# Performance work log

Hardware: AMD Instinct MI355X
Metric: run time of the kernel (lower is better)

The kernel has to match this reference:

```python
import jax, jax.numpy as jnp
import numpy as np

N = 50000
E = 800000
IN_DIM, HID_DIM, LAT_DIM, OUT_DIM = 128, 128, 64, 128
NEG_SLOPE = 0.2  # PyG GATConv default


def setup_inputs() -> dict:
    key = jax.random.key(0)
    ks = jax.random.split(key, 24)
    def glorot(k, shape):
        lim = float(np.sqrt(6.0 / (shape[0] + shape[-1])))
        return jax.random.uniform(k, shape, jnp.float32, -lim, lim)
    inp = {
        "x": jax.random.normal(ks[0], (N, IN_DIM), jnp.float32),
        "edge_index": jax.random.randint(ks[1], (2, E), 0, N, jnp.int32),
        "eps": jax.random.normal(ks[2], (N, LAT_DIM), jnp.float32),
        # GATConv 1 (heads=1)
        "W1": glorot(ks[3], (IN_DIM, HID_DIM)),
        "a_src1": glorot(ks[4], (HID_DIM,)),
        "a_dst1": glorot(ks[5], (HID_DIM,)),
        "b1": jnp.zeros((HID_DIM,), jnp.float32),
        # GATConv 2
        "W2": glorot(ks[6], (HID_DIM, LAT_DIM)),
        "a_src2": glorot(ks[7], (LAT_DIM,)),
        "a_dst2": glorot(ks[8], (LAT_DIM,)),
        "b2": jnp.zeros((LAT_DIM,), jnp.float32),
        # VAE heads
        "W_mu": glorot(ks[9], (LAT_DIM, LAT_DIM)),
        "b_mu": jnp.zeros((LAT_DIM,), jnp.float32),
        "W_lv": glorot(ks[10], (LAT_DIM, LAT_DIM)),
        "b_lv": jnp.zeros((LAT_DIM,), jnp.float32),
        "W_d1": glorot(ks[11], (LAT_DIM, HID_DIM)),
        "b_d1": jnp.zeros((HID_DIM,), jnp.float32),
        "W_d2": glorot(ks[12], (HID_DIM, OUT_DIM)),
        "b_d2": jnp.zeros((OUT_DIM,), jnp.float32),
    }
    return inp


def gat_conv(x, W, a_src, a_dst, b, src, dst):
    # x: [N, F_in] -> h: [N, F_out]
    h = x @ W
    # per-node attention halves (single head)
    alpha_s = h @ a_src           # [N]
    alpha_d = h @ a_dst           # [N]
    # per-edge score: leaky_relu(a_src . h_j + a_dst . h_i), edge j->i
    e = jax.nn.leaky_relu(alpha_s[src] + alpha_d[dst], NEG_SLOPE)  # [E']
    # scatter-softmax over incoming edges of each destination node
    m = jax.ops.segment_max(e, dst, num_segments=N)                # [N]
    ex = jnp.exp(e - m[dst])
    denom = jax.ops.segment_sum(ex, dst, num_segments=N)           # [N]
    w = ex / denom[dst]                                            # [E']
    # scatter-add weighted messages
    out = jax.ops.segment_sum(h[src] * w[:, None], dst, num_segments=N)
    return out + b


def reference(x, edge_index, eps, W1, a_src1, a_dst1, b1, W2, a_src2, a_dst2, b2,
              W_mu, b_mu, W_lv, b_lv, W_d1, b_d1, W_d2, b_d2):
    # add self loops (PyG GATConv default add_self_loops=True)
    loops = jnp.arange(N, dtype=edge_index.dtype)
    src = jnp.concatenate([edge_index[0], loops])
    dst = jnp.concatenate([edge_index[1], loops])

    h = jax.nn.relu(gat_conv(x, W1, a_src1, a_dst1, b1, src, dst))
    h = jax.nn.relu(gat_conv(h, W2, a_src2, a_dst2, b2, src, dst))
    mu = h @ W_mu + b_mu
    logvar = h @ W_lv + b_lv
    z = mu + eps * jnp.exp(0.5 * logvar)
    d = jax.nn.relu(z @ W_d1 + b_d1)
    recon_x = jax.nn.sigmoid(d @ W_d2 + b_d2)
    return recon_x, mu, logvar
```

## Files before the change

### kernel.cpp

```cpp
#include <hip/hip_runtime.h>
#include <stdint.h>

typedef unsigned int u32;

__device__ __forceinline__ float lrelu(float x){ return x > 0.f ? x : 0.2f*x; }

__global__ void k_hist(const int* __restrict__ dst, int* __restrict__ deg, int E){
  int e = blockIdx.x*blockDim.x + threadIdx.x;
  if (e < E) atomicAdd(&deg[dst[e]], 1);
}

__global__ void k_scan1(const int* __restrict__ deg, int* __restrict__ offs,
                        int* __restrict__ bsum, int n){
  __shared__ int lds[256];
  int t = threadIdx.x;
  int base = blockIdx.x*1024 + t*4;
  int v0 = (base+0<n)?deg[base+0]:0;
  int v1 = (base+1<n)?deg[base+1]:0;
  int v2 = (base+2<n)?deg[base+2]:0;
  int v3 = (base+3<n)?deg[base+3]:0;
  int s = v0+v1+v2+v3;
  lds[t] = s; __syncthreads();
  for (int off=1; off<256; off<<=1){
    int tmp = (t>=off)? lds[t-off] : 0;
    __syncthreads();
    lds[t] += tmp;
    __syncthreads();
  }
  int excl = lds[t] - s;
  if (t==255) bsum[blockIdx.x] = lds[255];
  if (base+0<n) offs[base+0] = excl;
  if (base+1<n) offs[base+1] = excl+v0;
  if (base+2<n) offs[base+2] = excl+v0+v1;
  if (base+3<n) offs[base+3] = excl+v0+v1+v2;
}

__global__ void k_scan2(int* bsum, int nb){
  int lane = threadIdx.x;
  int v = (lane<nb)? bsum[lane] : 0;
  int orig = v;
  for (int off=1; off<64; off<<=1){
    int t = __shfl_up(v, off);
    if (lane >= off) v += t;
  }
  if (lane<nb) bsum[lane] = v - orig;
}

__global__ void k_scan3(int* __restrict__ offs, int* __restrict__ cur,
                        const int* __restrict__ bsum, int n){
  int i = blockIdx.x*blockDim.x + threadIdx.x;
  if (i<n){ int v = offs[i] + bsum[i>>10]; offs[i]=v; cur[i]=v; }
}

__global__ void k_scatter(const int* __restrict__ src, const int* __restrict__ dst,
                          int* __restrict__ cur, int* __restrict__ adj, int E){
  int e = blockIdx.x*blockDim.x + threadIdx.x;
  if (e<E){
    int d = dst[e];
    int p = atomicAdd(&cur[d], 1);
    adj[p] = src[e];
  }
}

template<int FOUT>
__global__ __launch_bounds__(256) void k_gemm_t(const float* __restrict__ X,
                                                const float* __restrict__ W,
                                                float* __restrict__ H, int N){
  constexpr int CG = FOUT/4;
  constexpr int RG = 256/CG;
  constexpr int TR = RG*4;
  __shared__ float xs[TR*128];
  __shared__ float ws[128*FOUT];
  int t = threadIdx.x;
  long i0 = (long)blockIdx.x * TR;
  {
    constexpr int NV = TR*32/256;
    #pragma unroll
    for (int j=0;j<NV;j++){
      int idx = t + 256*j;
      int row = idx >> 5, c4 = idx & 31;
      float4 v = make_float4(0.f,0.f,0.f,0.f);
      if (i0 + row < N) v = *(const float4*)&X[(i0+row)*128 + c4*4];
      *(float4*)&xs[row*128 + c4*4] = v;
    }
  }
  {
    constexpr int NW = 128*FOUT/4/256;
    const float4* Wv = (const float4*)W;
    float4* wd = (float4*)ws;
    #pragma unroll
    for (int j=0;j<NW;j++) wd[t + 256*j] = Wv[t + 256*j];
  }
  __syncthreads();
  int ci = t & (CG-1), rg = t / CG;
  float4 a0 = make_float4(0,0,0,0), a1 = a0, a2 = a0, a3 = a0;
  const float* xrow = &xs[(rg*4)*128];
  #pragma unroll 8
  for (int k=0;k<128;k++){
    float4 w4 = *(const float4*)&ws[k*FOUT + ci*4];
    float x0 = xrow[k];
    float x1 = xrow[128 + k];
    float x2 = xrow[256 + k];
    float x3 = xrow[384 + k];
    a0.x = fmaf(x0, w4.x, a0.x); a0.y = fmaf(x0, w4.y, a0.y);
    a0.z = fmaf(x0, w4.z, a0.z); a0.w = fmaf(x0, w4.w, a0.w);
    a1.x = fmaf(x1, w4.x, a1.x); a1.y = fmaf(x1, w4.y, a1.y);
    a1.z = fmaf(x1, w4.z, a1.z); a1.w = fmaf(x1, w4.w, a1.w);
    a2.x = fmaf(x2, w4.x, a2.x); a2.y = fmaf(x2, w4.y, a2.y);
    a2.z = fmaf(x2, w4.z, a2.z); a2.w = fmaf(x2, w4.w, a2.w);
    a3.x = fmaf(x3, w4.x, a3.x); a3.y = fmaf(x3, w4.y, a3.y);
    a3.z = fmaf(x3, w4.z, a3.z); a3.w = fmaf(x3, w4.w, a3.w);
  }
  long ib = i0 + rg*4;
  if (ib+0 < N) *(float4*)&H[(ib+0)*FOUT + ci*4] = a0;
  if (ib+1 < N) *(float4*)&H[(ib+1)*FOUT + ci*4] = a1;
  if (ib+2 < N) *(float4*)&H[(ib+2)*FOUT + ci*4] = a2;
  if (ib+3 < N) *(float4*)&H[(ib+3)*FOUT + ci*4] = a3;
}

template<int F>
__global__ void k_alpha(const float* __restrict__ H, const float* __restrict__ Asrc,
                        const float* __restrict__ Adst, float* __restrict__ AS,
                        float* __restrict__ AD, int N){
  int lane = threadIdx.x & 63;
  int i = blockIdx.x*4 + (threadIdx.x >> 6);
  if (i >= N) return;
  float as = 0.f, ad = 0.f;
  #pragma unroll
  for (int c = lane; c < F; c += 64){
    float hv = H[(long)i*F + c];
    as = fmaf(hv, Asrc[c], as);
    ad = fmaf(hv, Adst[c], ad);
  }
  #pragma unroll
  for (int off=32; off; off>>=1){
    as += __shfl_xor(as, off);
    ad += __shfl_xor(ad, off);
  }
  if (lane==0){ AS[i]=as; AD[i]=ad; }
}

template<int F>
__global__ void k_agg(const float* __restrict__ H, const float* __restrict__ AS,
                      const float* __restrict__ AD, const float* __restrict__ B,
                      const int* __restrict__ offs, const int* __restrict__ deg,
                      const int* __restrict__ adj, float* __restrict__ OUT, int N){
  int lane = threadIdx.x & 63;
  int i = blockIdx.x*4 + (threadIdx.x >> 6);
  if (i >= N) return;
  int start = offs[i], dg = deg[i];
  float ad = AD[i];
  float lr_self = lrelu(AS[i] + ad);
  float m = -1e30f, dacc = 0.f;
  for (int b0=0; b0<dg; b0+=64){
    int k = b0 + lane;
    if (k < dg){
      int s = adj[start+k];
      float lr = lrelu(AS[s] + ad);
      float mn = fmaxf(m, lr);
      dacc = dacc*__expf(m-mn) + __expf(lr-mn);
      m = mn;
    }
  }
  #pragma unroll
  for (int off=32; off; off>>=1){
    float m2 = __shfl_xor(m, off);
    float d2 = __shfl_xor(dacc, off);
    float mn = fmaxf(m, m2);
    dacc = dacc*__expf(m-mn) + d2*__expf(m2-mn);
    m = mn;
  }
  float M = fmaxf(m, lr_self);
  float D = dacc*__expf(m-M) + __expf(lr_self-M);
  float invD = 1.f/D;
  float wself = __expf(lr_self-M)*invD;
  float acc0 = wself * H[(long)i*F + lane];
  float acc1 = 0.f;
  if (F==128) acc1 = wself * H[(long)i*F + 64 + lane];
  for (int b0=0; b0<dg; b0+=64){
    int k = b0 + lane;
    int sreg = 0; float wreg = 0.f;
    if (k < dg){
      sreg = adj[start+k];
      wreg = __expf(lrelu(AS[sreg]+ad) - M)*invD;
    }
    int cnt = min(64, dg-b0);
    int kk = 0;
    for (; kk+4<=cnt; kk+=4){
      int   s0=__shfl(sreg,kk),   s1=__shfl(sreg,kk+1),   s2=__shfl(sreg,kk+2),   s3=__shfl(sreg,kk+3);
      float w0=__shfl(wreg,kk),   w1=__shfl(wreg,kk+1),   w2=__shfl(wreg,kk+2),   w3=__shfl(wreg,kk+3);
      float h0 = H[(long)s0*F+lane];
      float h1 = H[(long)s1*F+lane];
      float h2 = H[(long)s2*F+lane];
      float h3 = H[(long)s3*F+lane];
      acc0 += w0*h0 + w1*h1 + w2*h2 + w3*h3;
      if (F==128){
        float g0 = H[(long)s0*F+64+lane];
        float g1 = H[(long)s1*F+64+lane];
        float g2 = H[(long)s2*F+64+lane];
        float g3 = H[(long)s3*F+64+lane];
        acc1 += w0*g0 + w1*g1 + w2*g2 + w3*g3;
      }
    }
    for (; kk<cnt; kk++){
      int s0=__shfl(sreg,kk); float w0=__shfl(wreg,kk);
      acc0 += w0*H[(long)s0*F+lane];
      if (F==128) acc1 += w0*H[(long)s0*F+64+lane];
    }
  }
  float o0 = fmaxf(acc0 + B[lane], 0.f);
  OUT[(long)i*F+lane] = o0;
  if (F==128){
    float o1 = fmaxf(acc1 + B[64+lane], 0.f);
    OUT[(long)i*F+64+lane] = o1;
  }
}

__global__ __launch_bounds__(512) void k_head_t(
    const float* __restrict__ H2, const float* __restrict__ EPS,
    const float* __restrict__ Wmu, const float* __restrict__ bmu,
    const float* __restrict__ Wlv, const float* __restrict__ blv,
    const float* __restrict__ Wd1, const float* __restrict__ bd1,
    const float* __restrict__ Wd2, const float* __restrict__ bd2,
    float* __restrict__ out_recon, float* __restrict__ out_mu,
    float* __restrict__ out_lv, int N){
  __shared__ float hs[64*64];
  __shared__ float zs[64*64];
  __shared__ float dsb[64*128];
  __shared__ float ws[128*128];
  int t = threadIdx.x;
  long i0 = (long)blockIdx.x * 64;
  #pragma unroll
  for (int j=0;j<2;j++){
    int idx = t + 512*j;
    int row = idx >> 4, c4 = idx & 15;
    float4 v = make_float4(0.f,0.f,0.f,0.f);
    if (i0 + row < N) v = *(const float4*)&H2[(i0+row)*64 + c4*4];
    *(float4*)&hs[row*64 + c4*4] = v;
  }
  #pragma unroll
  for (int j=0;j<4;j++){
    int q = t + 512*j;
    int k = q >> 5, c4 = q & 31;
    float4 v;
    if (c4 < 16) v = *(const float4*)&Wmu[k*64 + c4*4];
    else         v = *(const float4*)&Wlv[k*64 + (c4-16)*4];
    *(float4*)&ws[k*128 + c4*4] = v;
  }
  __syncthreads();
  int ci = t & 31, rg = t >> 5;
  float4 a0 = make_float4(0,0,0,0), a1 = a0, a2 = a0, a3 = a0;
  {
    const float* xrow = &hs[(rg*4)*64];
    #pragma unroll 8
    for (int k=0;k<64;k++){
      float4 w4 = *(const float4*)&ws[k*128 + ci*4];
      float x0 = xrow[k], x1 = xrow[64+k], x2 = xrow[128+k], x3 = xrow[192+k];
      a0.x=fmaf(x0,w4.x,a0.x); a0.y=fmaf(x0,w4.y,a0.y); a0.z=fmaf(x0,w4.z,a0.z); a0.w=fmaf(x0,w4.w,a0.w);
      a1.x=fmaf(x1,w4.x,a1.x); a1.y=fmaf(x1,w4.y,a1.y); a1.z=fmaf(x1,w4.z,a1.z); a1.w=fmaf(x1,w4.w,a1.w);
      a2.x=fmaf(x2,w4.x,a2.x); a2.y=fmaf(x2,w4.y,a2.y); a2.z=fmaf(x2,w4.z,a2.z); a2.w=fmaf(x2,w4.w,a2.w);
      a3.x=fmaf(x3,w4.x,a3.x); a3.y=fmaf(x3,w4.y,a3.y); a3.z=fmaf(x3,w4.z,a3.z); a3.w=fmaf(x3,w4.w,a3.w);
    }
  }
  bool is_mu = (ci < 16);
  int cbase = is_mu ? ci*4 : (ci-16)*4;
  if (!is_mu){
    float4 bv = *(const float4*)&blv[cbase];
    float4 acc[4] = {a0,a1,a2,a3};
    #pragma unroll
    for (int r=0;r<4;r++){
      long i = i0 + rg*4 + r;
      float4 lv = make_float4(acc[r].x+bv.x, acc[r].y+bv.y, acc[r].z+bv.z, acc[r].w+bv.w);
      if (i < N) *(float4*)&out_lv[i*64 + cbase] = lv;
      *(float4*)&zs[(rg*4+r)*64 + cbase] = lv;
    }
  }
  __syncthreads();
  if (is_mu){
    float4 bv = *(const float4*)&bmu[cbase];
    float4 acc[4] = {a0,a1,a2,a3};
    #pragma unroll
    for (int r=0;r<4;r++){
      long i = i0 + rg*4 + r;
      float4 mu = make_float4(acc[r].x+bv.x, acc[r].y+bv.y, acc[r].z+bv.z, acc[r].w+bv.w);
      if (i < N) *(float4*)&out_mu[i*64 + cbase] = mu;
      float4 lv = *(const float4*)&zs[(rg*4+r)*64 + cbase];
      float4 e = make_float4(0.f,0.f,0.f,0.f);
      if (i < N) e = *(const float4*)&EPS[i*64 + cbase];
      float4 z;
      z.x = fmaf(e.x, __expf(0.5f*lv.x), mu.x);
      z.y = fmaf(e.y, __expf(0.5f*lv.y), mu.y);
      z.z = fmaf(e.z, __expf(0.5f*lv.z), mu.z);
      z.w = fmaf(e.w, __expf(0.5f*lv.w), mu.w);
      *(float4*)&zs[(rg*4+r)*64 + cbase] = z;
    }
  }
  {
    const float4* Wv = (const float4*)Wd1;
    float4* wd = (float4*)ws;
    #pragma unroll
    for (int j=0;j<4;j++) wd[t + 512*j] = Wv[t + 512*j];
  }
  __syncthreads();
  a0 = make_float4(0,0,0,0); a1 = a0; a2 = a0; a3 = a0;
  {
    const float* xrow = &zs[(rg*4)*64];
    #pragma unroll 8
    for (int k=0;k<64;k++){
      float4 w4 = *(const float4*)&ws[k*128 + ci*4];
      float x0 = xrow[k], x1 = xrow[64+k], x2 = xrow[128+k], x3 = xrow[192+k];
      a0.x=fmaf(x0,w4.x,a0.x); a0.y=fmaf(x0,w4.y,a0.y); a0.z=fmaf(x0,w4.z,a0.z); a0.w=fmaf(x0,w4.w,a0.w);
      a1.x=fmaf(x1,w4.x,a1.x); a1.y=fmaf(x1,w4.y,a1.y); a1.z=fmaf(x1,w4.z,a1.z); a1.w=fmaf(x1,w4.w,a1.w);
      a2.x=fmaf(x2,w4.x,a2.x); a2.y=fmaf(x2,w4.y,a2.y); a2.z=fmaf(x2,w4.z,a2.z); a2.w=fmaf(x2,w4.w,a2.w);
      a3.x=fmaf(x3,w4.x,a3.x); a3.y=fmaf(x3,w4.y,a3.y); a3.z=fmaf(x3,w4.z,a3.z); a3.w=fmaf(x3,w4.w,a3.w);
    }
  }
  __syncthreads();
  {
    float4 bv = *(const float4*)&bd1[ci*4];
    float4 acc[4] = {a0,a1,a2,a3};
    #pragma unroll
    for (int r=0;r<4;r++){
      float4 d;
      d.x = fmaxf(acc[r].x+bv.x, 0.f); d.y = fmaxf(acc[r].y+bv.y, 0.f);
      d.z = fmaxf(acc[r].z+bv.z, 0.f); d.w = fmaxf(acc[r].w+bv.w, 0.f);
      *(float4*)&dsb[(rg*4+r)*128 + ci*4] = d;
    }
  }
  {
    const float4* Wv = (const float4*)Wd2;
    float4* wd = (float4*)ws;
    #pragma unroll
    for (int j=0;j<8;j++) wd[t + 512*j] = Wv[t + 512*j];
  }
  __syncthreads();
  a0 = make_float4(0,0,0,0); a1 = a0; a2 = a0; a3 = a0;
  {
    const float* xrow = &dsb[(rg*4)*128];
    #pragma unroll 8
    for (int k=0;k<128;k++){
      float4 w4 = *(const float4*)&ws[k*128 + ci*4];
      float x0 = xrow[k], x1 = xrow[128+k], x2 = xrow[256+k], x3 = xrow[384+k];
      a0.x=fmaf(x0,w4.x,a0.x); a0.y=fmaf(x0,w4.y,a0.y); a0.z=fmaf(x0,w4.z,a0.z); a0.w=fmaf(x0,w4.w,a0.w);
      a1.x=fmaf(x1,w4.x,a1.x); a1.y=fmaf(x1,w4.y,a1.y); a1.z=fmaf(x1,w4.z,a1.z); a1.w=fmaf(x1,w4.w,a1.w);
      a2.x=fmaf(x2,w4.x,a2.x); a2.y=fmaf(x2,w4.y,a2.y); a2.z=fmaf(x2,w4.z,a2.z); a2.w=fmaf(x2,w4.w,a2.w);
      a3.x=fmaf(x3,w4.x,a3.x); a3.y=fmaf(x3,w4.y,a3.y); a3.z=fmaf(x3,w4.z,a3.z); a3.w=fmaf(x3,w4.w,a3.w);
    }
  }
  {
    float4 bv = *(const float4*)&bd2[ci*4];
    float4 acc[4] = {a0,a1,a2,a3};
    #pragma unroll
    for (int r=0;r<4;r++){
      long i = i0 + rg*4 + r;
      if (i < N){
        float4 o;
        o.x = 1.f/(1.f+__expf(-(acc[r].x+bv.x)));
        o.y = 1.f/(1.f+__expf(-(acc[r].y+bv.y)));
        o.z = 1.f/(1.f+__expf(-(acc[r].z+bv.z)));
        o.w = 1.f/(1.f+__expf(-(acc[r].w+bv.w)));
        *(float4*)&out_recon[i*128 + ci*4] = o;
      }
    }
  }
}

extern "C" void kernel_launch(void* const* d_in, const int* in_sizes, int n_in,
                              void* d_out, int out_size, void* d_ws, size_t ws_size,
                              hipStream_t stream){
  const float* x    = (const float*)d_in[0];
  const int*   ei   = (const int*)  d_in[1];
  const float* eps  = (const float*)d_in[2];
  const float* W1   = (const float*)d_in[3];
  const float* as1v = (const float*)d_in[4];
  const float* ad1v = (const float*)d_in[5];
  const float* b1   = (const float*)d_in[6];
  const float* W2   = (const float*)d_in[7];
  const float* as2v = (const float*)d_in[8];
  const float* ad2v = (const float*)d_in[9];
  const float* b2   = (const float*)d_in[10];
  const float* Wmu  = (const float*)d_in[11];
  const float* bmu  = (const float*)d_in[12];
  const float* Wlv  = (const float*)d_in[13];
  const float* blv  = (const float*)d_in[14];
  const float* Wd1  = (const float*)d_in[15];
  const float* bd1  = (const float*)d_in[16];
  const float* Wd2  = (const float*)d_in[17];
  const float* bd2  = (const float*)d_in[18];

  const int N = in_sizes[0] / 128;
  const int E = in_sizes[1] / 2;
  const int* esrc = ei;
  const int* edst = ei + E;

  char* wp = (char*)d_ws;
  auto alloc = [&](size_t bytes)->char*{
    char* p = wp; wp += (bytes + 255) & ~(size_t)255; return p;
  };
  int*   deg  = (int*)  alloc((size_t)N*4);
  int*   offs = (int*)  alloc((size_t)N*4);
  int*   cur  = (int*)  alloc((size_t)N*4);
  int*   bsum = (int*)  alloc(256*4);
  int*   adj  = (int*)  alloc((size_t)E*4);
  float* h1   = (float*)alloc((size_t)N*128*4);
  float* o1   = (float*)alloc((size_t)N*128*4);
  float* AS1  = (float*)alloc((size_t)N*4);
  float* AD1  = (float*)alloc((size_t)N*4);
  float* AS2  = (float*)alloc((size_t)N*4);
  float* AD2  = (float*)alloc((size_t)N*4);
  float* h2 = h1;
  float* o2 = h1 + (size_t)N*64;
  (void)ws_size; (void)n_in; (void)out_size;

  float* out_recon = (float*)d_out;
  float* out_mu    = out_recon + (size_t)N*128;
  float* out_lv    = out_mu    + (size_t)N*64;

  hipMemsetAsync(deg, 0, (size_t)N*4, stream);
  int eb = (E + 255)/256;
  int nb = (N + 1023)/1024;
  k_hist   <<<eb, 256, 0, stream>>>(edst, deg, E);
  k_scan1  <<<nb, 256, 0, stream>>>(deg, offs, bsum, N);
  k_scan2  <<<1,   64, 0, stream>>>(bsum, nb);
  k_scan3  <<<(N+255)/256, 256, 0, stream>>>(offs, cur, bsum, N);
  k_scatter<<<eb, 256, 0, stream>>>(esrc, edst, cur, adj, E);

  int wb  = (N+3)/4;
  int gb1 = (N+31)/32;
  int gb2 = (N+63)/64;
  int hb  = (N+63)/64;
  k_gemm_t<128><<<gb1, 256, 0, stream>>>(x, W1, h1, N);
  k_alpha<128> <<<wb, 256, 0, stream>>>(h1, as1v, ad1v, AS1, AD1, N);
  k_agg<128>   <<<wb, 256, 0, stream>>>(h1, AS1, AD1, b1, offs, deg, adj, o1, N);
  k_gemm_t<64> <<<gb2, 256, 0, stream>>>(o1, W2, h2, N);
  k_alpha<64>  <<<wb, 256, 0, stream>>>(h2, as2v, ad2v, AS2, AD2, N);
  k_agg<64>    <<<wb, 256, 0, stream>>>(h2, AS2, AD2, b2, offs, deg, adj, o2, N);
  k_head_t     <<<hb, 512, 0, stream>>>(o2, eps, Wmu, bmu, Wlv, blv, Wd1, bd1, Wd2, bd2,
                                        out_recon, out_mu, out_lv, N);
}
```

Before: 445.4 us.

## Fuse attention logits into GEMM, vectorize aggregation, drop LDS weight staging

The per-node attention dot products move into the GEMM epilogue through shuffle reductions, which removes both alpha kernels. The GEMMs and the head kernel now read weights straight from global or cache instead of staging them in LDS, and each thread computes more rows. Aggregation gains a single-pass softmax for nodes with degree up to 64 and processes several edges per wavefront with float4 lanes, reducing across lane partitions at the end. The trade-offs are higher register pressure and weight reads that now depend on cache behaviour.

```diff
diff --git a/kernel.cpp b/kernel.cpp
--- a/kernel.cpp
+++ b/kernel.cpp
@@ -62,161 +62,166 @@
   }
 }
 
-template<int FOUT>
-__global__ __launch_bounds__(256) void k_gemm_t(const float* __restrict__ X,
-                                                const float* __restrict__ W,
-                                                float* __restrict__ H, int N){
+template<int FOUT, int RPT>
+__global__ __launch_bounds__(256) void k_gemm2(const float* __restrict__ X,
+    const float* __restrict__ W, const float* __restrict__ Avs,
+    const float* __restrict__ Avd, float* __restrict__ H,
+    float* __restrict__ AS, float* __restrict__ AD, int N){
   constexpr int CG = FOUT/4;
   constexpr int RG = 256/CG;
-  constexpr int TR = RG*4;
+  constexpr int TR = RG*RPT;
   __shared__ float xs[TR*128];
-  __shared__ float ws[128*FOUT];
   int t = threadIdx.x;
   long i0 = (long)blockIdx.x * TR;
-  {
-    constexpr int NV = TR*32/256;
-    #pragma unroll
-    for (int j=0;j<NV;j++){
-      int idx = t + 256*j;
-      int row = idx >> 5, c4 = idx & 31;
-      float4 v = make_float4(0.f,0.f,0.f,0.f);
-      if (i0 + row < N) v = *(const float4*)&X[(i0+row)*128 + c4*4];
-      *(float4*)&xs[row*128 + c4*4] = v;
-    }
-  }
-  {
-    constexpr int NW = 128*FOUT/4/256;
-    const float4* Wv = (const float4*)W;
-    float4* wd = (float4*)ws;
-    #pragma unroll
-    for (int j=0;j<NW;j++) wd[t + 256*j] = Wv[t + 256*j];
+  #pragma unroll
+  for (int j=0;j<TR*128/4/256;j++){
+    int idx = t + 256*j;
+    int row = idx >> 5, c4 = idx & 31;
+    float4 v = make_float4(0.f,0.f,0.f,0.f);
+    if (i0 + row < N) v = *(const float4*)&X[(i0+row)*128 + c4*4];
+    *(float4*)&xs[row*128 + c4*4] = v;
   }
   __syncthreads();
   int ci = t & (CG-1), rg = t / CG;
-  float4 a0 = make_float4(0,0,0,0), a1 = a0, a2 = a0, a3 = a0;
-  const float* xrow = &xs[(rg*4)*128];
-  #pragma unroll 8
+  const float* Wc = W + ci*4;
+  float4 acc[RPT];
+  #pragma unroll
+  for (int r=0;r<RPT;r++) acc[r] = make_float4(0.f,0.f,0.f,0.f);
+  const float* xrow = &xs[(rg*RPT)*128];
+  #pragma unroll 4
   for (int k=0;k<128;k++){
-    float4 w4 = *(const float4*)&ws[k*FOUT + ci*4];
-    float x0 = xrow[k];
-    float x1 = xrow[128 + k];
-    float x2 = xrow[256 + k];
-    float x3 = xrow[384 + k];
-    a0.x = fmaf(x0, w4.x, a0.x); a0.y = fmaf(x0, w4.y, a0.y);
-    a0.z = fmaf(x0, w4.z, a0.z); a0.w = fmaf(x0, w4.w, a0.w);
-    a1.x = fmaf(x1, w4.x, a1.x); a1.y = fmaf(x1, w4.y, a1.y);
-    a1.z = fmaf(x1, w4.z, a1.z); a1.w = fmaf(x1, w4.w, a1.w);
-    a2.x = fmaf(x2, w4.x, a2.x); a2.y = fmaf(x2, w4.y, a2.y);
-    a2.z = fmaf(x2, w4.z, a2.z); a2.w = fmaf(x2, w4.w, a2.w);
-    a3.x = fmaf(x3, w4.x, a3.x); a3.y = fmaf(x3, w4.y, a3.y);
-    a3.z = fmaf(x3, w4.z, a3.z); a3.w = fmaf(x3, w4.w, a3.w);
-  }
-  long ib = i0 + rg*4;
-  if (ib+0 < N) *(float4*)&H[(ib+0)*FOUT + ci*4] = a0;
-  if (ib+1 < N) *(float4*)&H[(ib+1)*FOUT + ci*4] = a1;
-  if (ib+2 < N) *(float4*)&H[(ib+2)*FOUT + ci*4] = a2;
-  if (ib+3 < N) *(float4*)&H[(ib+3)*FOUT + ci*4] = a3;
+    float4 w4 = *(const float4*)&Wc[k*FOUT];
+    #pragma unroll
+    for (int r=0;r<RPT;r++){
+      float xv = xrow[r*128 + k];
+      acc[r].x = fmaf(xv, w4.x, acc[r].x);
+      acc[r].y = fmaf(xv, w4.y, acc[r].y);
+      acc[r].z = fmaf(xv, w4.z, acc[r].z);
+      acc[r].w = fmaf(xv, w4.w, acc[r].w);
+    }
+  }
+  float4 vs = *(const float4*)&Avs[ci*4];
+  float4 vd = *(const float4*)&Avd[ci*4];
+  float asv[RPT], adv[RPT];
+  #pragma unroll
+  for (int r=0;r<RPT;r++){
+    asv[r] = acc[r].x*vs.x + acc[r].y*vs.y + acc[r].z*vs.z + acc[r].w*vs.w;
+    adv[r] = acc[r].x*vd.x + acc[r].y*vd.y + acc[r].z*vd.z + acc[r].w*vd.w;
+  }
+  #pragma unroll
+  for (int off=1; off<CG; off<<=1){
+    #pragma unroll
+    for (int r=0;r<RPT;r++){
+      asv[r] += __shfl_xor(asv[r], off);
+      adv[r] += __shfl_xor(adv[r], off);
+    }
+  }
+  long rb = i0 + rg*RPT;
+  #pragma unroll
+  for (int r=0;r<RPT;r++)
+    if (rb + r < N) *(float4*)&H[(rb+r)*FOUT + ci*4] = acc[r];
+  if (ci == 0){
+    #pragma unroll
+    for (int r=0;r<RPT;r++)
+      if (rb + r < N){ AS[rb+r] = asv[r]; AD[rb+r] = adv[r]; }
+  }
 }
 
 template<int F>
-__global__ void k_alpha(const float* __restrict__ H, const float* __restrict__ Asrc,
-                        const float* __restrict__ Adst, float* __restrict__ AS,
-                        float* __restrict__ AD, int N){
-  int lane = threadIdx.x & 63;
-  int i = blockIdx.x*4 + (threadIdx.x >> 6);
-  if (i >= N) return;
-  float as = 0.f, ad = 0.f;
-  #pragma unroll
-  for (int c = lane; c < F; c += 64){
-    float hv = H[(long)i*F + c];
-    as = fmaf(hv, Asrc[c], as);
-    ad = fmaf(hv, Adst[c], ad);
-  }
-  #pragma unroll
-  for (int off=32; off; off>>=1){
-    as += __shfl_xor(as, off);
-    ad += __shfl_xor(ad, off);
-  }
-  if (lane==0){ AS[i]=as; AD[i]=ad; }
-}
-
-template<int F>
-__global__ void k_agg(const float* __restrict__ H, const float* __restrict__ AS,
-                      const float* __restrict__ AD, const float* __restrict__ B,
-                      const int* __restrict__ offs, const int* __restrict__ deg,
-                      const int* __restrict__ adj, float* __restrict__ OUT, int N){
+__global__ __launch_bounds__(256) void k_agg2(const float* __restrict__ H,
+    const float* __restrict__ AS, const float* __restrict__ AD,
+    const float* __restrict__ B, const int* __restrict__ offs,
+    const int* __restrict__ deg, const int* __restrict__ adj,
+    float* __restrict__ OUT, int N){
+  constexpr int PL = F/4;
+  constexpr int PARTS = 64/PL;
   int lane = threadIdx.x & 63;
   int i = blockIdx.x*4 + (threadIdx.x >> 6);
   if (i >= N) return;
   int start = offs[i], dg = deg[i];
   float ad = AD[i];
   float lr_self = lrelu(AS[i] + ad);
-  float m = -1e30f, dacc = 0.f;
+  int part = lane / PL, lp = lane % PL;
+  float M, invD, wfast = 0.f;
+  int sfast = i;
+  if (dg <= 64){
+    float lr = -1e30f;
+    if (lane < dg){ sfast = adj[start+lane]; lr = lrelu(AS[sfast] + ad); }
+    float m = lr;
+    #pragma unroll
+    for (int off=32; off; off>>=1) m = fmaxf(m, __shfl_xor(m, off));
+    M = fmaxf(m, lr_self);
+    float p = (lane < dg) ? __expf(lr - M) : 0.f;
+    float d = p;
+    #pragma unroll
+    for (int off=32; off; off>>=1) d += __shfl_xor(d, off);
+    invD = 1.f/(d + __expf(lr_self - M));
+    wfast = p * invD;
+  } else {
+    float m = -1e30f, dacc = 0.f;
+    for (int b0=0; b0<dg; b0+=64){
+      int k = b0 + lane;
+      if (k < dg){
+        int s = adj[start+k];
+        float lr = lrelu(AS[s] + ad);
+        float mn = fmaxf(m, lr);
+        dacc = dacc*__expf(m-mn) + __expf(lr-mn);
+        m = mn;
+      }
+    }
+    #pragma unroll
+    for (int off=32; off; off>>=1){
+      float m2 = __shfl_xor(m, off);
+      float d2 = __shfl_xor(dacc, off);
+      float mn = fmaxf(m, m2);
+      dacc = dacc*__expf(m-mn) + d2*__expf(m2-mn);
+      m = mn;
+    }
+    M = fmaxf(m, lr_self);
+    invD = 1.f/(dacc*__expf(m-M) + __expf(lr_self-M));
+  }
+  float4 acc = make_float4(0.f,0.f,0.f,0.f);
+  if (part == 0){
+    float ws_ = __expf(lr_self - M)*invD;
+    float4 hv = *(const float4*)&H[(long)i*F + lp*4];
+    acc.x = ws_*hv.x; acc.y = ws_*hv.y; acc.z = ws_*hv.z; acc.w = ws_*hv.w;
+  }
   for (int b0=0; b0<dg; b0+=64){
-    int k = b0 + lane;
-    if (k < dg){
-      int s = adj[start+k];
-      float lr = lrelu(AS[s] + ad);
-      float mn = fmaxf(m, lr);
-      dacc = dacc*__expf(m-mn) + __expf(lr-mn);
-      m = mn;
-    }
-  }
-  #pragma unroll
-  for (int off=32; off; off>>=1){
-    float m2 = __shfl_xor(m, off);
-    float d2 = __shfl_xor(dacc, off);
-    float mn = fmaxf(m, m2);
-    dacc = dacc*__expf(m-mn) + d2*__expf(m2-mn);
-    m = mn;
-  }
-  float M = fmaxf(m, lr_self);
-  float D = dacc*__expf(m-M) + __expf(lr_self-M);
-  float invD = 1.f/D;
-  float wself = __expf(lr_self-M)*invD;
-  float acc0 = wself * H[(long)i*F + lane];
-  float acc1 = 0.f;
-  if (F==128) acc1 = wself * H[(long)i*F + 64 + lane];
-  for (int b0=0; b0<dg; b0+=64){
-    int k = b0 + lane;
-    int sreg = 0; float wreg = 0.f;
-    if (k < dg){
-      sreg = adj[start+k];
-      wreg = __expf(lrelu(AS[sreg]+ad) - M)*invD;
-    }
-    int cnt = min(64, dg-b0);
-    int kk = 0;
-    for (; kk+4<=cnt; kk+=4){
-      int   s0=__shfl(sreg,kk),   s1=__shfl(sreg,kk+1),   s2=__shfl(sreg,kk+2),   s3=__shfl(sreg,kk+3);
-      float w0=__shfl(wreg,kk),   w1=__shfl(wreg,kk+1),   w2=__shfl(wreg,kk+2),   w3=__shfl(wreg,kk+3);
-      float h0 = H[(long)s0*F+lane];
-      float h1 = H[(long)s1*F+lane];
-      float h2 = H[(long)s2*F+lane];
-      float h3 = H[(long)s3*F+lane];
-      acc0 += w0*h0 + w1*h1 + w2*h2 + w3*h3;
-      if (F==128){
-        float g0 = H[(long)s0*F+64+lane];
-        float g1 = H[(long)s1*F+64+lane];
-        float g2 = H[(long)s2*F+64+lane];
-        float g3 = H[(long)s3*F+64+lane];
-        acc1 += w0*g0 + w1*g1 + w2*g2 + w3*g3;
-      }
-    }
-    for (; kk<cnt; kk++){
-      int s0=__shfl(sreg,kk); float w0=__shfl(wreg,kk);
-      acc0 += w0*H[(long)s0*F+lane];
-      if (F==128) acc1 += w0*H[(long)s0*F+64+lane];
-    }
-  }
-  float o0 = fmaxf(acc0 + B[lane], 0.f);
-  OUT[(long)i*F+lane] = o0;
-  if (F==128){
-    float o1 = fmaxf(acc1 + B[64+lane], 0.f);
-    OUT[(long)i*F+64+lane] = o1;
-  }
-}
-
-__global__ __launch_bounds__(512) void k_head_t(
+    int s_; float w_;
+    if (dg <= 64){ s_ = sfast; w_ = wfast; }
+    else {
+      s_ = i; w_ = 0.f;
+      int k = b0 + lane;
+      if (k < dg){ s_ = adj[start+k]; w_ = __expf(lrelu(AS[s_]+ad) - M)*invD; }
+    }
+    int cnt = min(64, dg - b0);
+    for (int kk=0; kk<cnt; kk += PARTS*4){
+      #pragma unroll
+      for (int j=0;j<4;j++){
+        int e = kk + j*PARTS + part;
+        int   s = __shfl(s_, e);
+        float w = __shfl(w_, e);
+        const float4 hv = *(const float4*)&H[(long)s*F + lp*4];
+        acc.x = fmaf(w, hv.x, acc.x); acc.y = fmaf(w, hv.y, acc.y);
+        acc.z = fmaf(w, hv.z, acc.z); acc.w = fmaf(w, hv.w, acc.w);
+      }
+    }
+  }
+  #pragma unroll
+  for (int off=PL; off<64; off<<=1){
+    acc.x += __shfl_xor(acc.x, off); acc.y += __shfl_xor(acc.y, off);
+    acc.z += __shfl_xor(acc.z, off); acc.w += __shfl_xor(acc.w, off);
+  }
+  if (part == 0){
+    float4 bv = *(const float4*)&B[lp*4];
+    float4 o;
+    o.x = fmaxf(acc.x+bv.x, 0.f); o.y = fmaxf(acc.y+bv.y, 0.f);
+    o.z = fmaxf(acc.z+bv.z, 0.f); o.w = fmaxf(acc.w+bv.w, 0.f);
+    *(float4*)&OUT[(long)i*F + lp*4] = o;
+  }
+}
+
+__global__ __launch_bounds__(256) void k_head2(
     const float* __restrict__ H2, const float* __restrict__ EPS,
     const float* __restrict__ Wmu, const float* __restrict__ bmu,
     const float* __restrict__ Wlv, const float* __restrict__ blv,
@@ -224,67 +229,60 @@
     const float* __restrict__ Wd2, const float* __restrict__ bd2,
     float* __restrict__ out_recon, float* __restrict__ out_mu,
     float* __restrict__ out_lv, int N){
-  __shared__ float hs[64*64];
-  __shared__ float zs[64*64];
-  __shared__ float dsb[64*128];
-  __shared__ float ws[128*128];
+  __shared__ float smem[64*128];
+  float* hs  = smem;
+  float* zs  = smem + 64*64;
+  float* dsb = smem;
   int t = threadIdx.x;
   long i0 = (long)blockIdx.x * 64;
   #pragma unroll
-  for (int j=0;j<2;j++){
-    int idx = t + 512*j;
+  for (int j=0;j<4;j++){
+    int idx = t + 256*j;
     int row = idx >> 4, c4 = idx & 15;
     float4 v = make_float4(0.f,0.f,0.f,0.f);
     if (i0 + row < N) v = *(const float4*)&H2[(i0+row)*64 + c4*4];
     *(float4*)&hs[row*64 + c4*4] = v;
   }
-  #pragma unroll
-  for (int j=0;j<4;j++){
-    int q = t + 512*j;
-    int k = q >> 5, c4 = q & 31;
-    float4 v;
-    if (c4 < 16) v = *(const float4*)&Wmu[k*64 + c4*4];
-    else         v = *(const float4*)&Wlv[k*64 + (c4-16)*4];
-    *(float4*)&ws[k*128 + c4*4] = v;
-  }
   __syncthreads();
   int ci = t & 31, rg = t >> 5;
-  float4 a0 = make_float4(0,0,0,0), a1 = a0, a2 = a0, a3 = a0;
+  bool is_mu = (ci < 16);
+  int cbase = (is_mu ? ci : ci-16)*4;
+  long rb = i0 + rg*8;
+  float4 acc[8];
+  #pragma unroll
+  for (int r=0;r<8;r++) acc[r] = make_float4(0.f,0.f,0.f,0.f);
   {
-    const float* xrow = &hs[(rg*4)*64];
-    #pragma unroll 8
+    const float* Wp = (is_mu ? Wmu : Wlv) + cbase;
+    const float* xrow = &hs[(rg*8)*64];
+    #pragma unroll 4
     for (int k=0;k<64;k++){
-      float4 w4 = *(const float4*)&ws[k*128 + ci*4];
-      float x0 = xrow[k], x1 = xrow[64+k], x2 = xrow[128+k], x3 = xrow[192+k];
-      a0.x=fmaf(x0,w4.x,a0.x); a0.y=fmaf(x0,w4.y,a0.y); a0.z=fmaf(x0,w4.z,a0.z); a0.w=fmaf(x0,w4.w,a0.w);
-      a1.x=fmaf(x1,w4.x,a1.x); a1.y=fmaf(x1,w4.y,a1.y); a1.z=fmaf(x1,w4.z,a1.z); a1.w=fmaf(x1,w4.w,a1.w);
-      a2.x=fmaf(x2,w4.x,a2.x); a2.y=fmaf(x2,w4.y,a2.y); a2.z=fmaf(x2,w4.z,a2.z); a2.w=fmaf(x2,w4.w,a2.w);
-      a3.x=fmaf(x3,w4.x,a3.x); a3.y=fmaf(x3,w4.y,a3.y); a3.z=fmaf(x3,w4.z,a3.z); a3.w=fmaf(x3,w4.w,a3.w);
-    }
-  }
-  bool is_mu = (ci < 16);
-  int cbase = is_mu ? ci*4 : (ci-16)*4;
+      float4 w4 = *(const float4*)&Wp[k*64];
+      #pragma unroll
+      for (int r=0;r<8;r++){
+        float xv = xrow[r*64 + k];
+        acc[r].x = fmaf(xv,w4.x,acc[r].x); acc[r].y = fmaf(xv,w4.y,acc[r].y);
+        acc[r].z = fmaf(xv,w4.z,acc[r].z); acc[r].w = fmaf(xv,w4.w,acc[r].w);
+      }
+    }
+  }
   if (!is_mu){
     float4 bv = *(const float4*)&blv[cbase];
-    float4 acc[4] = {a0,a1,a2,a3};
-    #pragma unroll
-    for (int r=0;r<4;r++){
-      long i = i0 + rg*4 + r;
+    #pragma unroll
+    for (int r=0;r<8;r++){
       float4 lv = make_float4(acc[r].x+bv.x, acc[r].y+bv.y, acc[r].z+bv.z, acc[r].w+bv.w);
-      if (i < N) *(float4*)&out_lv[i*64 + cbase] = lv;
-      *(float4*)&zs[(rg*4+r)*64 + cbase] = lv;
+      if (rb + r < N) *(float4*)&out_lv[(rb+r)*64 + cbase] = lv;
+      *(float4*)&zs[(rg*8+r)*64 + cbase] = lv;
     }
   }
   __syncthreads();
   if (is_mu){
     float4 bv = *(const float4*)&bmu[cbase];
-    float4 acc[4] = {a0,a1,a2,a3};
-    #pragma unroll
-    for (int r=0;r<4;r++){
-      long i = i0 + rg*4 + r;
+    #pragma unroll
+    for (int r=0;r<8;r++){
+      long i = rb + r;
       float4 mu = make_float4(acc[r].x+bv.x, acc[r].y+bv.y, acc[r].z+bv.z, acc[r].w+bv.w);
       if (i < N) *(float4*)&out_mu[i*64 + cbase] = mu;
-      float4 lv = *(const float4*)&zs[(rg*4+r)*64 + cbase];
+      float4 lv = *(const float4*)&zs[(rg*8+r)*64 + cbase];
       float4 e = make_float4(0.f,0.f,0.f,0.f);
       if (i < N) e = *(const float4*)&EPS[i*64 + cbase];
       float4 z;
@@ -292,67 +290,59 @@
       z.y = fmaf(e.y, __expf(0.5f*lv.y), mu.y);
       z.z = fmaf(e.z, __expf(0.5f*lv.z), mu.z);
       z.w = fmaf(e.w, __expf(0.5f*lv.w), mu.w);
-      *(float4*)&zs[(rg*4+r)*64 + cbase] = z;
-    }
-  }
+      *(float4*)&zs[(rg*8+r)*64 + cbase] = z;
+    }
+  }
+  __syncthreads();
+  #pragma unroll
+  for (int r=0;r<8;r++) acc[r] = make_float4(0.f,0.f,0.f,0.f);
   {
-    const float4* Wv = (const float4*)Wd1;
-    float4* wd = (float4*)ws;
-    #pragma unroll
-    for (int j=0;j<4;j++) wd[t + 512*j] = Wv[t + 512*j];
-  }
-  __syncthreads();
-  a0 = make_float4(0,0,0,0); a1 = a0; a2 = a0; a3 = a0;
-  {
-    const float* xrow = &zs[(rg*4)*64];
-    #pragma unroll 8
+    const float* Wp = Wd1 + ci*4;
+    const float* xrow = &zs[(rg*8)*64];
+    #pragma unroll 4
     for (int k=0;k<64;k++){
-      float4 w4 = *(const float4*)&ws[k*128 + ci*4];
-      float x0 = xrow[k], x1 = xrow[64+k], x2 = xrow[128+k], x3 = xrow[192+k];
-      a0.x=fmaf(x0,w4.x,a0.x); a0.y=fmaf(x0,w4.y,a0.y); a0.z=fmaf(x0,w4.z,a0.z); a0.w=fmaf(x0,w4.w,a0.w);
-      a1.x=fmaf(x1,w4.x,a1.x); a1.y=fmaf(x1,w4.y,a1.y); a1.z=fmaf(x1,w4.z,a1.z); a1.w=fmaf(x1,w4.w,a1.w);
-      a2.x=fmaf(x2,w4.x,a2.x); a2.y=fmaf(x2,w4.y,a2.y); a2.z=fmaf(x2,w4.z,a2.z); a2.w=fmaf(x2,w4.w,a2.w);
-      a3.x=fmaf(x3,w4.x,a3.x); a3.y=fmaf(x3,w4.y,a3.y); a3.z=fmaf(x3,w4.z,a3.z); a3.w=fmaf(x3,w4.w,a3.w);
+      float4 w4 = *(const float4*)&Wp[k*128];
+      #pragma unroll
+      for (int r=0;r<8;r++){
+        float xv = xrow[r*64 + k];
+        acc[r].x = fmaf(xv,w4.x,acc[r].x); acc[r].y = fmaf(xv,w4.y,acc[r].y);
+        acc[r].z = fmaf(xv,w4.z,acc[r].z); acc[r].w = fmaf(xv,w4.w,acc[r].w);
+      }
     }
   }
   __syncthreads();
   {
     float4 bv = *(const float4*)&bd1[ci*4];
-    float4 acc[4] = {a0,a1,a2,a3};
-    #pragma unroll
-    for (int r=0;r<4;r++){
+    #pragma unroll
+    for (int r=0;r<8;r++){
       float4 d;
       d.x = fmaxf(acc[r].x+bv.x, 0.f); d.y = fmaxf(acc[r].y+bv.y, 0.f);
       d.z = fmaxf(acc[r].z+bv.z, 0.f); d.w = fmaxf(acc[r].w+bv.w, 0.f);
-      *(float4*)&dsb[(rg*4+r)*128 + ci*4] = d;
-    }
-  }
+      *(float4*)&dsb[(rg*8+r)*128 + ci*4] = d;
+    }
+  }
+  __syncthreads();
+  #pragma unroll
+  for (int r=0;r<8;r++) acc[r] = make_float4(0.f,0.f,0.f,0.f);
   {
-    const float4* Wv = (const float4*)Wd2;
-    float4* wd = (float4*)ws;
-    #pragma unroll
-    for (int j=0;j<8;j++) wd[t + 512*j] = Wv[t + 512*j];
-  }
-  __syncthreads();
-  a0 = make_float4(0,0,0,0); a1 = a0; a2 = a0; a3 = a0;
-  {
-    const float* xrow = &dsb[(rg*4)*128];
-    #pragma unroll 8
+    const float* Wp = Wd2 + ci*4;
+    const float* xrow = &dsb[(rg*8)*128];
+    #pragma unroll 2
     for (int k=0;k<128;k++){
-      float4 w4 = *(const float4*)&ws[k*128 + ci*4];
-      float x0 = xrow[k], x1 = xrow[128+k], x2 = xrow[256+k], x3 = xrow[384+k];
-      a0.x=fmaf(x0,w4.x,a0.x); a0.y=fmaf(x0,w4.y,a0.y); a0.z=fmaf(x0,w4.z,a0.z); a0.w=fmaf(x0,w4.w,a0.w);
-      a1.x=fmaf(x1,w4.x,a1.x); a1.y=fmaf(x1,w4.y,a1.y); a1.z=fmaf(x1,w4.z,a1.z); a1.w=fmaf(x1,w4.w,a1.w);
-      a2.x=fmaf(x2,w4.x,a2.x); a2.y=fmaf(x2,w4.y,a2.y); a2.z=fmaf(x2,w4.z,a2.z); a2.w=fmaf(x2,w4.w,a2.w);
-      a3.x=fmaf(x3,w4.x,a3.x); a3.y=fmaf(x3,w4.y,a3.y); a3.z=fmaf(x3,w4.z,a3.z); a3.w=fmaf(x3,w4.w,a3.w);
+      float4 w4 = *(const float4*)&Wp[k*128];
+      #pragma unroll
+      for (int r=0;r<8;r++){
+        float xv = xrow[r*128 + k];
+        acc[r].x = fmaf(xv,w4.x,acc[r].x); acc[r].y = fmaf(xv,w4.y,acc[r].y);
+        acc[r].z = fmaf(xv,w4.z,acc[r].z); acc[r].w = fmaf(xv,w4.w,acc[r].w);
+      }
     }
   }
   {
     float4 bv = *(const float4*)&bd2[ci*4];
-    float4 acc[4] = {a0,a1,a2,a3};
-    #pragma unroll
-    for (int r=0;r<4;r++){
-      long i = i0 + rg*4 + r;
+    #pragma unroll
+    for (int r=0;r<8;r++){
+      long i = rb + r;
       if (i < N){
         float4 o;
         o.x = 1.f/(1.f+__expf(-(acc[r].x+bv.x)));
@@ -425,16 +415,12 @@
   k_scan3  <<<(N+255)/256, 256, 0, stream>>>(offs, cur, bsum, N);
   k_scatter<<<eb, 256, 0, stream>>>(esrc, edst, cur, adj, E);
 
-  int wb  = (N+3)/4;
-  int gb1 = (N+31)/32;
-  int gb2 = (N+63)/64;
-  int hb  = (N+63)/64;
-  k_gemm_t<128><<<gb1, 256, 0, stream>>>(x, W1, h1, N);
-  k_alpha<128> <<<wb, 256, 0, stream>>>(h1, as1v, ad1v, AS1, AD1, N);
-  k_agg<128>   <<<wb, 256, 0, stream>>>(h1, AS1, AD1, b1, offs, deg, adj, o1, N);
-  k_gemm_t<64> <<<gb2, 256, 0, stream>>>(o1, W2, h2, N);
-  k_alpha<64>  <<<wb, 256, 0, stream>>>(h2, as2v, ad2v, AS2, AD2, N);
-  k_agg<64>    <<<wb, 256, 0, stream>>>(h2, AS2, AD2, b2, offs, deg, adj, o2, N);
-  k_head_t     <<<hb, 512, 0, stream>>>(o2, eps, Wmu, bmu, Wlv, blv, Wd1, bd1, Wd2, bd2,
-                                        out_recon, out_mu, out_lv, N);
-}
+  int wb = (N+3)/4;
+  int gb = (N+63)/64;
+  k_gemm2<128,8><<<gb, 256, 0, stream>>>(x,  W1, as1v, ad1v, h1, AS1, AD1, N);
+  k_agg2<128>   <<<wb, 256, 0, stream>>>(h1, AS1, AD1, b1, offs, deg, adj, o1, N);
+  k_gemm2<64,4> <<<gb, 256, 0, stream>>>(o1, W2, as2v, ad2v, h2, AS2, AD2, N);
+  k_agg2<64>    <<<wb, 256, 0, stream>>>(h2, AS2, AD2, b2, offs, deg, adj, o2, N);
+  k_head2       <<<gb, 256, 0, stream>>>(o2, eps, Wmu, bmu, Wlv, blv, Wd1, bd1, Wd2, bd2,
+                                         out_recon, out_mu, out_lv, N);
+}
```

Measured after the change: 423.4 us. 5.0% less time.
